# Optimization experiments

Hardware: AMD Instinct MI355X
Metric: run time of the kernel (lower is better)

The kernel has to match this reference:

```python
import jax, jax.numpy as jnp
import numpy as np

H, D_HEAD, MEM, K_OUT, J_DIM = 4, 16, 64, 192, 256
LN_EPS = 1e-5

def setup_inputs() -> dict:
    key = jax.random.key(0)
    ks = jax.random.split(key, 12)
    B, T, P = 4, 2048, 16
    inp = {
        "joint_repr": jax.random.normal(ks[0], (B, T, P, J_DIM), jnp.float32),
        "curvature": jax.random.uniform(ks[1], (B,), jnp.float32),
        "entropy": jax.random.uniform(ks[2], (B,), jnp.float32),
        "Wq": 0.02 * jax.random.normal(ks[3], (MEM, J_DIM), jnp.float32),
        "Wk": 0.02 * jax.random.normal(ks[4], (MEM, J_DIM), jnp.float32),
        "Wv": 0.02 * jax.random.normal(ks[5], (MEM, J_DIM), jnp.float32),
        "Wbeta_w": 0.05 * jax.random.normal(ks[6], (H, J_DIM), jnp.float32),
        "Wbeta_b": jnp.full((H,), 0.5, jnp.float32),
        "Walpha_w": 0.05 * jax.random.normal(ks[7], (H, J_DIM), jnp.float32),
        "Walpha_b": jnp.full((H,), -1.0, jnp.float32),
        "curv_w": 0.001 * jax.random.normal(ks[8], (H, 1), jnp.float32),
        "ent_w": 0.001 * jax.random.normal(ks[9], (H, 1), jnp.float32),
        "out_w": 0.01 * jax.random.normal(ks[10], (K_OUT, MEM), jnp.float32),
        "out_b": jnp.zeros((K_OUT,), jnp.float32),
        "ln_q_w": jnp.ones((D_HEAD,), jnp.float32),
        "ln_q_b": jnp.zeros((D_HEAD,), jnp.float32),
        "ln_k_w": jnp.ones((D_HEAD,), jnp.float32),
        "ln_k_b": jnp.zeros((D_HEAD,), jnp.float32),
    }
    return inp

def _ln(y, w, b):
    m = jnp.mean(y, axis=-1, keepdims=True)
    var = jnp.mean((y - m) ** 2, axis=-1, keepdims=True)
    return (y - m) / jnp.sqrt(var + LN_EPS) * w + b

def reference(joint_repr, curvature, entropy, Wq, Wk, Wv, Wbeta_w, Wbeta_b,
              Walpha_w, Walpha_b, curv_w, ent_w, out_w, out_b,
              ln_q_w, ln_q_b, ln_k_w, ln_k_b):
    B, T, P, J = joint_repr.shape
    N = B * P
    x = joint_repr.reshape(N, T, J)  # matches torch reshape(B*P, T, J)
    q = _ln((x @ Wq.T).reshape(N, T, H, D_HEAD), ln_q_w, ln_q_b)
    k = _ln((x @ Wk.T).reshape(N, T, H, D_HEAD), ln_k_w, ln_k_b)
    v = (x @ Wv.T).reshape(N, T, H, D_HEAD)
    k = k / jnp.clip(jnp.linalg.norm(k, axis=-1, keepdims=True), 1e-12)
    beta = jax.nn.sigmoid(x @ Wbeta_w.T + Wbeta_b)    # (N,T,H)
    alpha = jax.nn.sigmoid(x @ Walpha_w.T + Walpha_b)  # (N,T,H)
    # curvature modulation (detached in original)
    Kv = jnp.clip(jnp.abs(jax.lax.stop_gradient(curvature)), None, 10.0)
    Kv = jnp.repeat(Kv, P)  # (N,)
    beta = jax.nn.sigmoid(beta + Kv[:, None, None] * curv_w[:, 0])
    # entropy modulation (detached)
    Sv = jnp.clip(jax.lax.stop_gradient(entropy), 0.0, 5.0)
    Sv = jnp.repeat(Sv, P)
    alpha = jax.nn.sigmoid(alpha + Sv[:, None, None] * ent_w[:, 0])

    def step(M, inps):
        k_t, v_t, q_t, b_t, a_t = inps  # (N,H,d), (N,H)
        Mk = jnp.einsum('nhij,nhj->nhi', M, k_t)
        outer_kk = Mk[..., :, None] * k_t[..., None, :]
        outer_vk = v_t[..., :, None] * k_t[..., None, :]
        M = M - a_t[:, :, None, None] * outer_kk + b_t[:, :, None, None] * outer_vk
        o = jnp.einsum('nhij,nhj->nhi', M, q_t)
        return M, o

    M0 = jnp.zeros((N, H, D_HEAD, D_HEAD), joint_repr.dtype)
    xs = (k.transpose(1, 0, 2, 3), v.transpose(1, 0, 2, 3), q.transpose(1, 0, 2, 3),
          beta.transpose(1, 0, 2), alpha.transpose(1, 0, 2))
    _, outs = jax.lax.scan(step, M0, xs)  # (T,N,H,d)
    out = outs.transpose(1, 0, 2, 3).reshape(N, T, H * D_HEAD)
    fib = out @ out_w.T + out_b  # (N,T,K)
    return fib.reshape(B, P, T, K_OUT).transpose(0, 2, 1, 3)  # (B,T,P,K)
```

## Files before the change

kernel.cpp:

```cpp
#include <hip/hip_runtime.h>

#define TDIM 2048
#define SEG 16
#define SEGLEN 128

typedef __attribute__((ext_vector_type(8))) short short8;
typedef __attribute__((ext_vector_type(4))) short short4v;
typedef __attribute__((ext_vector_type(4))) float float4v;

__device__ __forceinline__ float sigf(float x) { return 1.0f / (1.0f + __expf(-x)); }

__device__ __forceinline__ unsigned short f2bf_rne(float f) {
    unsigned u = __float_as_uint(f);
    unsigned r = (u + 0x7fffu + ((u >> 16) & 1u)) >> 16;
    return (unsigned short)r;
}
__device__ __forceinline__ float bf2f(unsigned short h) {
    return __uint_as_float(((unsigned)h) << 16);
}
struct bfpair { short hi, lo; };
__device__ __forceinline__ bfpair cvt_split(float x) {
    bfpair p;
    unsigned short h = f2bf_rne(x);
    p.hi = (short)h;
    p.lo = (short)f2bf_rne(x - bf2f(h));
    return p;
}

__device__ __forceinline__ void split4_fast(float4 v, short4v& hi, short4v& lo) {
    unsigned h01, h23;
    asm("v_cvt_pk_bf16_f32 %0, %1, %2" : "=v"(h01) : "v"(v.x), "v"(v.y));
    asm("v_cvt_pk_bf16_f32 %0, %1, %2" : "=v"(h23) : "v"(v.z), "v"(v.w));
    float rx = v.x - __uint_as_float(h01 << 16);
    float ry = v.y - __uint_as_float(h01 & 0xffff0000u);
    float rz = v.z - __uint_as_float(h23 << 16);
    float rw = v.w - __uint_as_float(h23 & 0xffff0000u);
    unsigned l01, l23;
    asm("v_cvt_pk_bf16_f32 %0, %1, %2" : "=v"(l01) : "v"(rx), "v"(ry));
    asm("v_cvt_pk_bf16_f32 %0, %1, %2" : "=v"(l23) : "v"(rz), "v"(rw));
    union { unsigned u[2]; short4v s; } uh, ul;
    uh.u[0] = h01; uh.u[1] = h23;
    ul.u[0] = l01; ul.u[1] = l23;
    hi = uh.s; lo = ul.s;
}

template<int CTRL>
__device__ __forceinline__ float dpp_addt(float v) {
    int t = __builtin_amdgcn_update_dpp(0, __float_as_int(v), CTRL, 0xf, 0xf, true);
    return v + __int_as_float(t);
}
__device__ __forceinline__ float red16d(float v) {
    v = dpp_addt<0xB1>(v);
    v = dpp_addt<0x4E>(v);
    v = dpp_addt<0x141>(v);
    v = dpp_addt<0x140>(v);
    return v;
}

__device__ __forceinline__ float dot4f(float4 a, float4 b) {
    return fmaf(a.w, b.w, fmaf(a.z, b.z, fmaf(a.y, b.y, a.x * b.x)));
}
__device__ __forceinline__ float red4g(float v) {
    v += __shfl_xor(v, 16);
    v += __shfl_xor(v, 32);
    return v;
}

__device__ __forceinline__ void gld16(const void* g, void* l) {
    __builtin_amdgcn_global_load_lds(
        (const __attribute__((address_space(1))) unsigned*)g,
        (__attribute__((address_space(3))) unsigned*)l, 16, 0, 0);
}

__global__ __launch_bounds__(256) void prep_w_kernel(
    const float* __restrict__ Wq, const float* __restrict__ Wk, const float* __restrict__ Wv,
    const float* __restrict__ Wbw, const float* __restrict__ Waw,
    short* __restrict__ wimg)
{
    int u = blockIdx.x * 256 + threadIdx.x;
    if (u >= 6656) return;
    int kc = u / 1664, rem = u % 1664;
    int rr = rem >> 3, gg = rem & 7;
    const float* wrow = nullptr;
    if (rr < 64)       wrow = Wq  + (size_t)rr * 256;
    else if (rr < 128) wrow = Wk  + (size_t)(rr - 64) * 256;
    else if (rr < 192) wrow = Wv  + (size_t)(rr - 128) * 256;
    else if (rr < 196) wrow = Wbw + (size_t)(rr - 192) * 256;
    else if (rr < 200) wrow = Waw + (size_t)(rr - 196) * 256;
    int usw = (2 * gg) ^ (rr & 7);
    short* dh = wimg + ((size_t)kc * 3328 + rr * 16 + usw) * 8;
    short* dl = wimg + ((size_t)kc * 3328 + rr * 16 + (usw ^ 1)) * 8;
#pragma unroll
    for (int s = 0; s < 8; ++s) {
        float v = wrow ? wrow[kc * 64 + gg * 8 + s] : 0.0f;
        bfpair p = cvt_split(v);
        dh[s] = p.hi; dl[s] = p.lo;
    }
}

__global__ __launch_bounds__(256) void prep_ow_kernel(
    const float* __restrict__ ow, short* __restrict__ owimg)
{
    int u = blockIdx.x * 256 + threadIdx.x;
    if (u >= 1536) return;
    int rr = u >> 3, gg = u & 7;
    int usw = (2 * gg) ^ (rr & 7);
    short* dh = owimg + ((size_t)rr * 16 + usw) * 8;
    short* dl = owimg + ((size_t)rr * 16 + (usw ^ 1)) * 8;
#pragma unroll
    for (int s = 0; s < 8; ++s) {
        bfpair p = cvt_split(ow[(size_t)rr * 64 + gg * 8 + s]);
        dh[s] = p.hi; dl[s] = p.lo;
    }
}

__global__ __launch_bounds__(256, 4) void proj_kernel(
    const float* __restrict__ x, const float* __restrict__ curv, const float* __restrict__ ent,
    const short* __restrict__ wimg,
    const float* __restrict__ Wbb, const float* __restrict__ Wab,
    const float* __restrict__ cw, const float* __restrict__ ew,
    const float* __restrict__ lnqw, const float* __restrict__ lnqb,
    const float* __restrict__ lnkw, const float* __restrict__ lnkb,
    float* __restrict__ q_ws, float* __restrict__ k_ws, float* __restrict__ v_ws,
    float* __restrict__ beta_ws, float* __restrict__ alpha_ws)
{
    __shared__ __align__(16) short xsh[64 * 64];
    __shared__ __align__(16) short wsh[1664 * 8];

    const int tid = threadIdx.x;
    const int lane = tid & 63, wv = tid >> 6;
    const int i16 = lane & 15, gq = lane >> 4, swz = i16 & 7;
    const int row0 = blockIdx.x * 64;
    const int ntbase = (wv == 0) ? 0 : (1 + 3 * wv);
    const int ntcnt  = (wv == 0) ? 4 : 3;

    float4v acc[4][4];
#pragma unroll
    for (int m = 0; m < 4; ++m)
#pragma unroll
        for (int nI = 0; nI < 4; ++nI) acc[m][nI] = (float4v){0.f, 0.f, 0.f, 0.f};

    float4 xr[2];
#pragma unroll
    for (int it = 0; it < 2; ++it) {
        int f = it * 256 + tid, rr = f >> 3, c4 = f & 7;
        xr[it] = *(const float4*)&x[(size_t)(row0 + rr) * 256 + c4 * 4];
    }

    for (int hc = 0; hc < 8; ++hc) {
        __builtin_amdgcn_s_barrier();
        const short* wk = wimg + (size_t)(hc >> 1) * 26624;
        const int hoff = (hc & 1) * 8;
#pragma unroll
        for (int it = 0; it < 7; ++it) {
            int f = it * 256 + tid;
            if (f < 1664) {
                int rr = f >> 3, uu = f & 7;
                gld16(wk + ((size_t)rr * 16 + hoff + uu) * 8, &wsh[f * 8]);
            }
        }
        asm volatile("" ::: "memory");
#pragma unroll
        for (int it = 0; it < 2; ++it) {
            int f = it * 256 + tid, rr = f >> 3, c4 = f & 7;
            short4v hi, lo;
            split4_fast(xr[it], hi, lo);
            int usw = (2 * (c4 >> 1)) ^ (rr & 7);
            *(short4v*)&xsh[rr * 64 + usw * 8 + (c4 & 1) * 4] = hi;
            *(short4v*)&xsh[rr * 64 + (usw ^ 1) * 8 + (c4 & 1) * 4] = lo;
        }
        if (hc < 7) {
#pragma unroll
            for (int it = 0; it < 2; ++it) {
                int f = it * 256 + tid, rr = f >> 3, c4 = f & 7;
                xr[it] = *(const float4*)&x[(size_t)(row0 + rr) * 256 + (hc + 1) * 32 + c4 * 4];
            }
            asm volatile("s_waitcnt vmcnt(2) lgkmcnt(0)" ::: "memory");
        } else {
            asm volatile("s_waitcnt vmcnt(0) lgkmcnt(0)" ::: "memory");
        }
        __builtin_amdgcn_s_barrier();
        const int uA = ((2 * gq) ^ swz) * 8;
        short8 ah[4], al[4];
#pragma unroll
        for (int m = 0; m < 4; ++m) {
            const int rb = (m * 16 + i16) * 64;
            ah[m] = *(const short8*)&xsh[rb + uA];
            al[m] = *(const short8*)&xsh[rb + (uA ^ 8)];
        }
#pragma unroll
        for (int nI = 0; nI < 4; ++nI) if (nI < ntcnt) {
            const int rowB = ((ntbase + nI) * 16 + i16) * 64;
            short8 bh = *(const short8*)&wsh[rowB + uA];
            short8 bl = *(const short8*)&wsh[rowB + (uA ^ 8)];
#pragma unroll
            for (int m = 0; m < 4; ++m) {
                acc[m][nI] = __builtin_amdgcn_mfma_f32_16x16x32_bf16(ah[m], bh, acc[m][nI], 0, 0, 0);
                acc[m][nI] = __builtin_amdgcn_mfma_f32_16x16x32_bf16(ah[m], bl, acc[m][nI], 0, 0, 0);
                acc[m][nI] = __builtin_amdgcn_mfma_f32_16x16x32_bf16(al[m], bh, acc[m][nI], 0, 0, 0);
            }
        }
    }

    const int c = i16;
    const float lnqw_c = lnqw[c], lnqb_c = lnqb[c];
    const float lnkw_c = lnkw[c], lnkb_c = lnkb[c];
    const int nblk = row0 >> 11;
    const float Kv = fminf(fabsf(curv[nblk >> 4]), 10.0f);
    const float Sv = fminf(fmaxf(ent[nblk >> 4], 0.0f), 5.0f);
#pragma unroll
    for (int nI = 0; nI < 4; ++nI) if (nI < ntcnt) {
        const int nt = ntbase + nI;
#pragma unroll
        for (int m = 0; m < 4; ++m) {
#pragma unroll
            for (int j = 0; j < 4; ++j) {
                const int grow = row0 + m * 16 + gq * 4 + j;
                const int n = grow >> 11, t = grow & 2047;
                float y = acc[m][nI][j];
                if (nt < 4) {
                    float s = red16d(y), s2 = red16d(y * y);
                    float mean = s * 0.0625f;
                    float var = s2 * 0.0625f - mean * mean;
                    float inv = rsqrtf(var + 1e-5f);
                    q_ws[((size_t)(n * 4 + nt) * TDIM + t) * 16 + c] = (y - mean) * inv * lnqw_c + lnqb_c;
                } else if (nt < 8) {
                    float s = red16d(y), s2 = red16d(y * y);
                    float mean = s * 0.0625f;
                    float var = s2 * 0.0625f - mean * mean;
                    float inv = rsqrtf(var + 1e-5f);
                    float kn = (y - mean) * inv * lnkw_c + lnkb_c;
                    float s3 = red16d(kn * kn);
                    kn = kn / fmaxf(sqrtf(s3), 1e-12f);
                    k_ws[((size_t)(n * 4 + (nt - 4)) * TDIM + t) * 16 + c] = kn;
                } else if (nt < 12) {
                    v_ws[((size_t)(n * 4 + (nt - 8)) * TDIM + t) * 16 + c] = y;
                } else {
                    if (c < 4)
                        beta_ws[(size_t)(n * 4 + c) * TDIM + t] = sigf(sigf(y + Wbb[c]) + Kv * cw[c]);
                    else if (c < 8) {
                        int h = c - 4;
                        alpha_ws[(size_t)(n * 4 + h) * TDIM + t] = sigf(sigf(y + Wab[h]) + Sv * ew[h]);
                    }
                }
            }
        }
    }
}

__global__ __launch_bounds__(64) void scan_p1_kernel(
    const float* __restrict__ k_ws, const float* __restrict__ v_ws,
    const float* __restrict__ beta_ws, const float* __restrict__ alpha_ws,
    float* __restrict__ pq_ws)
{
    __shared__ __align__(16) float ks[128 * 16], bvs[128 * 16];
    __shared__ __align__(16) float tb1[128 * 4];
    const int tid = threadIdx.x;
    const int sid = blockIdx.x;
    const int cid = blockIdx.y;
    const int i = tid & 15, g = tid >> 4;
    const int t0g = sid * SEGLEN;
    const float* kb = k_ws + ((size_t)cid * TDIM + t0g) * 16;
    const float* vb = v_ws + ((size_t)cid * TDIM + t0g) * 16;
    const float* bb = beta_ws + (size_t)cid * TDIM + t0g;
    const float* ab = alpha_ws + (size_t)cid * TDIM + t0g;

    for (int f = tid; f < 128 * 16; f += 64) { ks[f] = 0.f; bvs[f] = 0.f; }
    for (int f = tid; f < 128 * 4; f += 64) tb1[f] = 0.f;
    __syncthreads();

    float4 kr[4], vr[4]; float be = 0.f, alp = 0.f;
    auto load_stage = [&](int s) {
        size_t t0 = (size_t)s * 64 + tid;
        const float4* kp = (const float4*)(kb + t0 * 16);
        const float4* vp = (const float4*)(vb + t0 * 16);
#pragma unroll
        for (int j = 0; j < 4; ++j) { kr[j] = kp[j]; vr[j] = vp[j]; }
        be = bb[t0]; alp = ab[t0];
    };
    auto commit_stage = [&](int s) {
        int r = (s & 1) * 64 + tid;
#pragma unroll
        for (int j = 0; j < 4; ++j) {
            *(float4*)&ks[r * 16 + 4 * j] = kr[j];
            float4 bv4 = make_float4(be * vr[j].x, be * vr[j].y, be * vr[j].z, be * vr[j].w);
            *(float4*)&bvs[r * 16 + 4 * j] = bv4;
        }
    };
    auto table_pass = [&](int s) {
        int r0 = (s & 1) * 64 + tid;
        int rm1 = (r0 - 1) & 127, rm2 = (r0 - 2) & 127;
        float C = 0.f, C2 = 0.f;
#pragma unroll
        for (int j = 0; j < 4; ++j) {
            float4 kt  = *(float4*)&ks[r0 * 16 + 4 * j];
            float4 km1 = *(float4*)&ks[rm1 * 16 + 4 * j];
            float4 km2 = *(float4*)&ks[rm2 * 16 + 4 * j];
            C  += dot4f(km1, kt);
            C2 += dot4f(km2, kt);
        }
        *(float4*)&tb1[r0 * 4] = make_float4(alp * C, alp * C2, alp, 0.f);
    };

    load_stage(0);
    commit_stage(0);
    __syncthreads();
    table_pass(0);
    __syncthreads();

    float4 Q4 = make_float4(0.f, 0.f, 0.f, 0.f);
    float4 P4 = make_float4(i == 4 * g + 0 ? 1.f : 0.f,
                            i == 4 * g + 1 ? 1.f : 0.f,
                            i == 4 * g + 2 ? 1.f : 0.f,
                            i == 4 * g + 3 ? 1.f : 0.f);
    float wq1 = 0.f, wq2 = 0.f, wp1 = 0.f, wp2 = 0.f;
    float4 k4m1 = make_float4(0.f, 0.f, 0.f, 0.f);
    float4 k4_0 = *(float4*)&ks[0 * 16 + 4 * g];
    float4 k4p1 = *(float4*)&ks[1 * 16 + 4 * g];
    float upQ_cur = 0.f;
    float upP_cur = ks[i];
    float4 ta0 = *(float4*)&tb1[0];
    float aC1_c = ta0.x, aC2_c = ta0.y, al_c = ta0.z;
    float bv_c = bvs[i];

    int t = 0;
    auto step = [&]() {
        int rp2 = (t + 2) & 127, rp1 = (t + 1) & 127;
        float4 k4in = *(float4*)&ks[rp2 * 16 + 4 * g];
        float4 tain = *(float4*)&tb1[rp1 * 4];
        float bvin = bvs[rp1 * 16 + i];
        float upQ = red4g(dot4f(Q4, k4p1));
        float upP = red4g(dot4f(P4, k4p1));
        Q4.x = fmaf(wq1, k4m1.x, Q4.x);
        Q4.y = fmaf(wq1, k4m1.y, Q4.y);
        Q4.z = fmaf(wq1, k4m1.z, Q4.z);
        Q4.w = fmaf(wq1, k4m1.w, Q4.w);
        P4.x = fmaf(wp1, k4m1.x, P4.x);
        P4.y = fmaf(wp1, k4m1.y, P4.y);
        P4.z = fmaf(wp1, k4m1.z, P4.z);
        P4.w = fmaf(wp1, k4m1.w, P4.w);
        float rq = fmaf(-aC2_c, wq2, fmaf(-al_c, upQ_cur, bv_c));
        float wq0 = fmaf(-aC1_c, wq1, rq);
        float rp_ = fmaf(-aC2_c, wp2, -al_c * upP_cur);
        float wp0 = fmaf(-aC1_c, wp1, rp_);
        wq2 = wq1; wq1 = wq0; wp2 = wp1; wp1 = wp0;
        k4m1 = k4_0; k4_0 = k4p1; k4p1 = k4in;
        upQ_cur = upQ; upP_cur = upP;
        aC1_c = tain.x; aC2_c = tain.y; al_c = tain.z; bv_c = bvin;
        ++t;
    };

    load_stage(1);
#pragma unroll 4
    for (int u = 0; u < 32; ++u) step();
    commit_stage(1);
#pragma unroll 4
    for (int u = 0; u < 16; ++u) step();
    table_pass(1);
#pragma unroll 4
    for (int u = 0; u < 16; ++u) step();
#pragma unroll 4
    for (int u = 0; u < 64; ++u) step();

    Q4.x = fmaf(wq1, k4m1.x, Q4.x);
    Q4.y = fmaf(wq1, k4m1.y, Q4.y);
    Q4.z = fmaf(wq1, k4m1.z, Q4.z);
    Q4.w = fmaf(wq1, k4m1.w, Q4.w);
    P4.x = fmaf(wp1, k4m1.x, P4.x);
    P4.y = fmaf(wp1, k4m1.y, P4.y);
    P4.z = fmaf(wp1, k4m1.z, P4.z);
    P4.w = fmaf(wp1, k4m1.w, P4.w);

    float* dst = pq_ws + ((size_t)cid * 15 + sid) * 512;
    *(float4*)&dst[i * 16 + 4 * g] = Q4;
    *(float4*)&dst[256 + i * 16 + 4 * g] = P4;
}

__global__ __launch_bounds__(64) void scan_p2_kernel(
    const float* __restrict__ pq_ws, float* __restrict__ min_ws)
{
    __shared__ float Mlds[256], Plds[256];
    const int tid = threadIdx.x;
    const int cid = blockIdx.x;
    const int i = tid & 15, g = tid >> 4;
    float4 M4 = make_float4(0.f, 0.f, 0.f, 0.f);
    *(float4*)&min_ws[((size_t)cid * SEG + 0) * 256 + i * 16 + 4 * g] = M4;
    for (int sid = 0; sid < 15; ++sid) {
        const float* base = pq_ws + ((size_t)cid * 15 + sid) * 512;
        float4 Qn = *(const float4*)&base[i * 16 + 4 * g];
        float4 Pn = *(const float4*)&base[256 + i * 16 + 4 * g];
        *(float4*)&Mlds[i * 16 + 4 * g] = M4;
        *(float4*)&Plds[i * 16 + 4 * g] = Pn;
        __syncthreads();
        float4 acc = Qn;
#pragma unroll
        for (int m = 0; m < 16; ++m) {
            float mm = Mlds[i * 16 + m];
            float4 pr = *(float4*)&Plds[m * 16 + 4 * g];
            acc.x = fmaf(mm, pr.x, acc.x);
            acc.y = fmaf(mm, pr.y, acc.y);
            acc.z = fmaf(mm, pr.z, acc.z);
            acc.w = fmaf(mm, pr.w, acc.w);
        }
        M4 = acc;
        __syncthreads();
        *(float4*)&min_ws[((size_t)cid * SEG + sid + 1) * 256 + i * 16 + 4 * g] = M4;
    }
}

__global__ __launch_bounds__(64) void scan_p3_kernel(
    const float* __restrict__ q_ws, const float* __restrict__ k_ws, const float* __restrict__ v_ws,
    const float* __restrict__ beta_ws, const float* __restrict__ alpha_ws,
    const float* __restrict__ min_ws, float* __restrict__ o_ws)
{
    __shared__ __align__(16) float ks[128 * 16], qs[128 * 16], bvs[128 * 16];
    __shared__ __align__(16) float tbl[128 * 8];
    __shared__ __align__(16) float os[64 * 16];
    const int tid = threadIdx.x;
    const int sid = blockIdx.x;
    const int cid = blockIdx.y;
    const int i = tid & 15, g = tid >> 4;
    const int t0g = sid * SEGLEN;
    const float* kb = k_ws + ((size_t)cid * TDIM + t0g) * 16;
    const float* qb = q_ws + ((size_t)cid * TDIM + t0g) * 16;
    const float* vb = v_ws + ((size_t)cid * TDIM + t0g) * 16;
    const float* bb = beta_ws + (size_t)cid * TDIM + t0g;
    const float* ab = alpha_ws + (size_t)cid * TDIM + t0g;
    float* obp = o_ws + ((size_t)cid * TDIM + t0g) * 16;

    for (int f = tid; f < 128 * 16; f += 64) { ks[f] = 0.f; qs[f] = 0.f; bvs[f] = 0.f; }
    for (int f = tid; f < 128 * 8; f += 64) tbl[f] = 0.f;
    __syncthreads();

    float4 kr[4], qr[4], vr[4]; float be = 0.f, alp = 0.f;
    auto load_stage = [&](int s) {
        size_t t0 = (size_t)s * 64 + tid;
        const float4* kp = (const float4*)(kb + t0 * 16);
        const float4* qp = (const float4*)(qb + t0 * 16);
        const float4* vp = (const float4*)(vb + t0 * 16);
#pragma unroll
        for (int j = 0; j < 4; ++j) { kr[j] = kp[j]; qr[j] = qp[j]; vr[j] = vp[j]; }
        be = bb[t0]; alp = ab[t0];
    };
    auto commit_stage = [&](int s) {
        int r = (s & 1) * 64 + tid;
#pragma unroll
        for (int j = 0; j < 4; ++j) {
            *(float4*)&ks[r * 16 + 4 * j] = kr[j];
            *(float4*)&qs[r * 16 + 4 * j] = qr[j];
            float4 bv4 = make_float4(be * vr[j].x, be * vr[j].y, be * vr[j].z, be * vr[j].w);
            *(float4*)&bvs[r * 16 + 4 * j] = bv4;
        }
    };
    auto table_pass = [&](int s) {
        int r0 = (s & 1) * 64 + tid;
        int rm1 = (r0 - 1) & 127, rm2 = (r0 - 2) & 127;
        float C = 0.f, C2 = 0.f, d = 0.f, e = 0.f, E2 = 0.f;
#pragma unroll
        for (int j = 0; j < 4; ++j) {
            float4 kt  = *(float4*)&ks[r0 * 16 + 4 * j];
            float4 km1 = *(float4*)&ks[rm1 * 16 + 4 * j];
            float4 km2 = *(float4*)&ks[rm2 * 16 + 4 * j];
            float4 qt  = *(float4*)&qs[r0 * 16 + 4 * j];
            C  += dot4f(km1, kt);
            C2 += dot4f(km2, kt);
            d  += dot4f(kt,  qt);
            e  += dot4f(km1, qt);
            E2 += dot4f(km2, qt);
        }
        *(float4*)&tbl[r0 * 8] = make_float4(alp * C, alp * C2, d, e);
        *(float2*)&tbl[r0 * 8 + 4] = make_float2(E2, alp);
    };

    load_stage(0);
    commit_stage(0);
    __syncthreads();
    table_pass(0);
    __syncthreads();

    float4 M4 = *(const float4*)&min_ws[((size_t)cid * SEG + sid) * 256 + i * 16 + 4 * g];
    float w1 = 0.f, w2 = 0.f;
    float4 k4m1 = make_float4(0.f, 0.f, 0.f, 0.f);
    float4 k4_0 = *(float4*)&ks[0 * 16 + 4 * g];
    float4 q4_0 = *(float4*)&qs[0 * 16 + 4 * g];
    float4 k4p1 = *(float4*)&ks[1 * 16 + 4 * g];
    float4 q4p1 = *(float4*)&qs[1 * 16 + 4 * g];
    float up_cur = red4g(dot4f(M4, k4_0));
    float rp_cur = red4g(dot4f(M4, q4_0));
    float4 ta0 = *(float4*)&tbl[0];
    float aC1_c = ta0.x, aC2_c = ta0.y, d_c = ta0.z, e_c = ta0.w;
    float2 tx0 = *(float2*)&tbl[4];
    float E2_c = tx0.x, al_c = tx0.y;
    float bv_c = bvs[i];

    int t = 0;
    auto step = [&]() {
        int rp2 = (t + 2) & 127, rp1 = (t + 1) & 127;
        float4 k4in = *(float4*)&ks[rp2 * 16 + 4 * g];
        float4 q4in = *(float4*)&qs[rp2 * 16 + 4 * g];
        float4 tain = *(float4*)&tbl[rp1 * 8];
        float2 txin = *(float2*)&tbl[rp1 * 8 + 4];
        float bvin = bvs[rp1 * 16 + i];
        float up = red4g(dot4f(M4, k4p1));
        float rp = red4g(dot4f(M4, q4p1));
        M4.x = fmaf(w1, k4m1.x, M4.x);
        M4.y = fmaf(w1, k4m1.y, M4.y);
        M4.z = fmaf(w1, k4m1.z, M4.z);
        M4.w = fmaf(w1, k4m1.w, M4.w);
        float r = fmaf(-aC2_c, w2, fmaf(-al_c, up_cur, bv_c));
        float w0 = fmaf(-aC1_c, w1, r);
        float o = fmaf(w0, d_c, fmaf(w1, e_c, fmaf(w2, E2_c, rp_cur)));
        if (g == 0) os[(t & 63) * 16 + i] = o;
        w2 = w1; w1 = w0;
        k4m1 = k4_0; k4_0 = k4p1; k4p1 = k4in;
        q4p1 = q4in;
        up_cur = up; rp_cur = rp;
        aC1_c = tain.x; aC2_c = tain.y; d_c = tain.z; e_c = tain.w;
        E2_c = txin.x; al_c = txin.y; bv_c = bvin;
        ++t;
    };

    for (int s = 0; s < 2; ++s) {
        if (s == 0) load_stage(1);
#pragma unroll 4
        for (int u = 0; u < 32; ++u) step();
        if (s == 0) commit_stage(1);
#pragma unroll 4
        for (int u = 0; u < 16; ++u) step();
        if (s == 0) table_pass(1);
#pragma unroll 4
        for (int u = 0; u < 16; ++u) step();
#pragma unroll
        for (int j = 0; j < 4; ++j) {
            float4 ov = *(float4*)&os[(tid * 4 + j) * 4];
            *(float4*)&obp[(size_t)s * 1024 + (tid * 4 + j) * 4] = ov;
        }
    }
}

__global__ __launch_bounds__(256, 4) void outproj_kernel(
    const float* __restrict__ o_ws, const short* __restrict__ owimg,
    const float* __restrict__ ob, float* __restrict__ out)
{
    __shared__ __align__(16) short osh[64 * 64];
    __shared__ __align__(16) short wsh[1536 * 8];
    const int tid = threadIdx.x;
    const int lane = tid & 63, wv = tid >> 6;
    const int i16 = lane & 15, gq = lane >> 4, swz = i16 & 7;
    const int row0 = blockIdx.x * 64;
    const int ntbase = wv * 3;

    float4v acc[4][3];
#pragma unroll
    for (int m = 0; m < 4; ++m)
#pragma unroll
        for (int nI = 0; nI < 3; ++nI) acc[m][nI] = (float4v){0.f, 0.f, 0.f, 0.f};

    float4 orr[2];
#pragma unroll
    for (int it = 0; it < 2; ++it) {
        int f = it * 256 + tid, rr = f >> 3, c4 = f & 7;
        int grow = row0 + rr;
        int n = grow >> 11, t = grow & 2047;
        int h = c4 >> 2, d4 = c4 & 3;
        orr[it] = *(const float4*)&o_ws[((size_t)(n * 4 + h) * TDIM + t) * 16 + d4 * 4];
    }

#pragma unroll
    for (int half = 0; half < 2; ++half) {
        __builtin_amdgcn_s_barrier();
#pragma unroll
        for (int it = 0; it < 6; ++it) {
            int f = it * 256 + tid;
            int rr = f >> 3, uu = f & 7;
            gld16(owimg + ((size_t)rr * 16 + half * 8 + uu) * 8, &wsh[f * 8]);
        }
        asm volatile("" ::: "memory");
#pragma unroll
        for (int it = 0; it < 2; ++it) {
            int f = it * 256 + tid, rr = f >> 3, c4 = f & 7;
            short4v hi, lo;
            split4_fast(orr[it], hi, lo);
            int usw = (2 * (c4 >> 1)) ^ (rr & 7);
            *(short4v*)&osh[rr * 64 + usw * 8 + (c4 & 1) * 4] = hi;
            *(short4v*)&osh[rr * 64 + (usw ^ 1) * 8 + (c4 & 1) * 4] = lo;
        }
        if (half == 0) {
#pragma unroll
            for (int it = 0; it < 2; ++it) {
                int f = it * 256 + tid, rr = f >> 3, c4 = f & 7;
                int grow = row0 + rr;
                int n = grow >> 11, t = grow & 2047;
                int col = 32 + c4 * 4;
                int h = col >> 4, d4 = (col >> 2) & 3;
                orr[it] = *(const float4*)&o_ws[((size_t)(n * 4 + h) * TDIM + t) * 16 + d4 * 4];
            }
            asm volatile("s_waitcnt vmcnt(2) lgkmcnt(0)" ::: "memory");
        } else {
            asm volatile("s_waitcnt vmcnt(0) lgkmcnt(0)" ::: "memory");
        }
        __builtin_amdgcn_s_barrier();

        const int uA = ((2 * gq) ^ swz) * 8;
        short8 ah[4], al[4];
#pragma unroll
        for (int m = 0; m < 4; ++m) {
            const int rb = (m * 16 + i16) * 64;
            ah[m] = *(const short8*)&osh[rb + uA];
            al[m] = *(const short8*)&osh[rb + (uA ^ 8)];
        }
#pragma unroll
        for (int nI = 0; nI < 3; ++nI) {
            const int rowB = ((ntbase + nI) * 16 + i16) * 64;
            short8 bh = *(const short8*)&wsh[rowB + uA];
            short8 bl = *(const short8*)&wsh[rowB + (uA ^ 8)];
#pragma unroll
            for (int m = 0; m < 4; ++m) {
                acc[m][nI] = __builtin_amdgcn_mfma_f32_16x16x32_bf16(ah[m], bh, acc[m][nI], 0, 0, 0);
                acc[m][nI] = __builtin_amdgcn_mfma_f32_16x16x32_bf16(ah[m], bl, acc[m][nI], 0, 0, 0);
                acc[m][nI] = __builtin_amdgcn_mfma_f32_16x16x32_bf16(al[m], bh, acc[m][nI], 0, 0, 0);
            }
        }
    }

#pragma unroll
    for (int nI = 0; nI < 3; ++nI) {
        const int nt = ntbase + nI;
        const float bias = ob[nt * 16 + i16];
#pragma unroll
        for (int m = 0; m < 4; ++m) {
#pragma unroll
            for (int j = 0; j < 4; ++j) {
                int grow = row0 + m * 16 + gq * 4 + j;
                int n = grow >> 11, t = grow & 2047;
                int b = n >> 4, p = n & 15;
                out[((size_t)(b * TDIM + t) * 16 + p) * 192 + nt * 16 + i16] = acc[m][nI][j] + bias;
            }
        }
    }
}

extern "C" void kernel_launch(void* const* d_in, const int* in_sizes, int n_in,
                              void* d_out, int out_size, void* d_ws, size_t ws_size,
                              hipStream_t stream) {
    (void)in_sizes; (void)n_in; (void)out_size; (void)ws_size;
    const float* x    = (const float*)d_in[0];
    const float* curv = (const float*)d_in[1];
    const float* ent  = (const float*)d_in[2];
    const float* Wq   = (const float*)d_in[3];
    const float* Wk   = (const float*)d_in[4];
    const float* Wv   = (const float*)d_in[5];
    const float* Wbw  = (const float*)d_in[6];
    const float* Wbb  = (const float*)d_in[7];
    const float* Waw  = (const float*)d_in[8];
    const float* Wab  = (const float*)d_in[9];
    const float* cw   = (const float*)d_in[10];
    const float* ew   = (const float*)d_in[11];
    const float* ow   = (const float*)d_in[12];
    const float* ob   = (const float*)d_in[13];
    const float* lnqw = (const float*)d_in[14];
    const float* lnqb = (const float*)d_in[15];
    const float* lnkw = (const float*)d_in[16];
    const float* lnkb = (const float*)d_in[17];
    float* out = (float*)d_out;

    float* ws = (float*)d_ws;
    float* q_ws     = ws;
    float* k_ws     = q_ws + 8388608;
    float* v_ws     = k_ws + 8388608;
    float* beta_ws  = v_ws + 8388608;
    float* alpha_ws = beta_ws + 524288;
    float* o_ws     = alpha_ws + 524288;

    short* wimg  = (short*)o_ws;
    short* owimg = (short*)q_ws;
    float* pq_ws  = out;
    float* min_ws = out + 1966080;

    prep_w_kernel<<<26, 256, 0, stream>>>(Wq, Wk, Wv, Wbw, Waw, wimg);
    proj_kernel<<<2048, 256, 0, stream>>>(x, curv, ent, wimg, Wbb, Wab,
                                          cw, ew, lnqw, lnqb, lnkw, lnkb,
                                          q_ws, k_ws, v_ws, beta_ws, alpha_ws);
    scan_p1_kernel<<<dim3(15, 256), 64, 0, stream>>>(k_ws, v_ws, beta_ws, alpha_ws, pq_ws);
    scan_p2_kernel<<<256, 64, 0, stream>>>(pq_ws, min_ws);
    scan_p3_kernel<<<dim3(16, 256), 64, 0, stream>>>(q_ws, k_ws, v_ws, beta_ws, alpha_ws,
                                                     min_ws, o_ws);
    prep_ow_kernel<<<6, 256, 0, stream>>>(ow, owimg);
    outproj_kernel<<<2048, 256, 0, stream>>>(o_ws, owimg, ob, out);
}
```

Measured before the change: 516.2 us.

## Halve scan segment length to 64 and double GEMM block rows to 128

The chunked delta-rule scan now splits the 2048-step sequence into 32 segments of 64 steps instead of 16 of 128. This doubles the number of parallel blocks in phases 1 and 3, halves the serial chain per block, and removes the two-stage load pipelining inside each segment, at the cost of a longer serial prefix combine in phase 2. Separately, the projection and output-projection GEMM kernels move to 512-thread blocks covering 128 rows, so each loaded weight tile is reused across two row groups of waves. Workspace offsets are adjusted to match the larger number of partial states.

```diff
diff --git a/kernel.cpp b/kernel.cpp
--- a/kernel.cpp
+++ b/kernel.cpp
@@ -1,8 +1,8 @@
 #include <hip/hip_runtime.h>
 
 #define TDIM 2048
-#define SEG 16
-#define SEGLEN 128
+#define SEGN 32
+#define SEGL 64
 
 typedef __attribute__((ext_vector_type(8))) short short8;
 typedef __attribute__((ext_vector_type(4))) short short4v;
@@ -114,7 +114,7 @@
     }
 }
 
-__global__ __launch_bounds__(256, 4) void proj_kernel(
+__global__ __launch_bounds__(512, 4) void proj_kernel(
     const float* __restrict__ x, const float* __restrict__ curv, const float* __restrict__ ent,
     const short* __restrict__ wimg,
     const float* __restrict__ Wbb, const float* __restrict__ Wab,
@@ -124,15 +124,16 @@
     float* __restrict__ q_ws, float* __restrict__ k_ws, float* __restrict__ v_ws,
     float* __restrict__ beta_ws, float* __restrict__ alpha_ws)
 {
-    __shared__ __align__(16) short xsh[64 * 64];
+    __shared__ __align__(16) short xsh[128 * 64];
     __shared__ __align__(16) short wsh[1664 * 8];
 
     const int tid = threadIdx.x;
     const int lane = tid & 63, wv = tid >> 6;
     const int i16 = lane & 15, gq = lane >> 4, swz = i16 & 7;
-    const int row0 = blockIdx.x * 64;
-    const int ntbase = (wv == 0) ? 0 : (1 + 3 * wv);
-    const int ntcnt  = (wv == 0) ? 4 : 3;
+    const int row0 = blockIdx.x * 128;
+    const int wr = wv >> 2, wc = wv & 3;
+    const int ntbase = (wc == 0) ? 0 : (1 + 3 * wc);
+    const int ntcnt  = (wc == 0) ? 4 : 3;
 
     float4v acc[4][4];
 #pragma unroll
@@ -143,7 +144,7 @@
     float4 xr[2];
 #pragma unroll
     for (int it = 0; it < 2; ++it) {
-        int f = it * 256 + tid, rr = f >> 3, c4 = f & 7;
+        int f = it * 512 + tid, rr = f >> 3, c4 = f & 7;
         xr[it] = *(const float4*)&x[(size_t)(row0 + rr) * 256 + c4 * 4];
     }
 
@@ -152,8 +153,8 @@
         const short* wk = wimg + (size_t)(hc >> 1) * 26624;
         const int hoff = (hc & 1) * 8;
 #pragma unroll
-        for (int it = 0; it < 7; ++it) {
-            int f = it * 256 + tid;
+        for (int it = 0; it < 4; ++it) {
+            int f = it * 512 + tid;
             if (f < 1664) {
                 int rr = f >> 3, uu = f & 7;
                 gld16(wk + ((size_t)rr * 16 + hoff + uu) * 8, &wsh[f * 8]);
@@ -162,7 +163,7 @@
         asm volatile("" ::: "memory");
 #pragma unroll
         for (int it = 0; it < 2; ++it) {
-            int f = it * 256 + tid, rr = f >> 3, c4 = f & 7;
+            int f = it * 512 + tid, rr = f >> 3, c4 = f & 7;
             short4v hi, lo;
             split4_fast(xr[it], hi, lo);
             int usw = (2 * (c4 >> 1)) ^ (rr & 7);
@@ -172,7 +173,7 @@
         if (hc < 7) {
 #pragma unroll
             for (int it = 0; it < 2; ++it) {
-                int f = it * 256 + tid, rr = f >> 3, c4 = f & 7;
+                int f = it * 512 + tid, rr = f >> 3, c4 = f & 7;
                 xr[it] = *(const float4*)&x[(size_t)(row0 + rr) * 256 + (hc + 1) * 32 + c4 * 4];
             }
             asm volatile("s_waitcnt vmcnt(2) lgkmcnt(0)" ::: "memory");
@@ -184,7 +185,7 @@
         short8 ah[4], al[4];
 #pragma unroll
         for (int m = 0; m < 4; ++m) {
-            const int rb = (m * 16 + i16) * 64;
+            const int rb = (wr * 64 + m * 16 + i16) * 64;
             ah[m] = *(const short8*)&xsh[rb + uA];
             al[m] = *(const short8*)&xsh[rb + (uA ^ 8)];
         }
@@ -215,7 +216,7 @@
         for (int m = 0; m < 4; ++m) {
 #pragma unroll
             for (int j = 0; j < 4; ++j) {
-                const int grow = row0 + m * 16 + gq * 4 + j;
+                const int grow = row0 + wr * 64 + m * 16 + gq * 4 + j;
                 const int n = grow >> 11, t = grow & 2047;
                 float y = acc[m][nI][j];
                 if (nt < 4) {
@@ -248,48 +249,46 @@
     }
 }
 
+
 __global__ __launch_bounds__(64) void scan_p1_kernel(
     const float* __restrict__ k_ws, const float* __restrict__ v_ws,
     const float* __restrict__ beta_ws, const float* __restrict__ alpha_ws,
     float* __restrict__ pq_ws)
 {
-    __shared__ __align__(16) float ks[128 * 16], bvs[128 * 16];
-    __shared__ __align__(16) float tb1[128 * 4];
+    __shared__ __align__(16) float ks[68 * 16], bvs[68 * 16];
+    __shared__ __align__(16) float tb1[68 * 4];
     const int tid = threadIdx.x;
     const int sid = blockIdx.x;
     const int cid = blockIdx.y;
     const int i = tid & 15, g = tid >> 4;
-    const int t0g = sid * SEGLEN;
+    const int t0g = sid * SEGL;
     const float* kb = k_ws + ((size_t)cid * TDIM + t0g) * 16;
     const float* vb = v_ws + ((size_t)cid * TDIM + t0g) * 16;
     const float* bb = beta_ws + (size_t)cid * TDIM + t0g;
     const float* ab = alpha_ws + (size_t)cid * TDIM + t0g;
 
-    for (int f = tid; f < 128 * 16; f += 64) { ks[f] = 0.f; bvs[f] = 0.f; }
-    for (int f = tid; f < 128 * 4; f += 64) tb1[f] = 0.f;
+    for (int f = tid; f < 68 * 16; f += 64) { ks[f] = 0.f; bvs[f] = 0.f; }
+    for (int f = tid; f < 68 * 4; f += 64) tb1[f] = 0.f;
     __syncthreads();
 
-    float4 kr[4], vr[4]; float be = 0.f, alp = 0.f;
-    auto load_stage = [&](int s) {
-        size_t t0 = (size_t)s * 64 + tid;
-        const float4* kp = (const float4*)(kb + t0 * 16);
-        const float4* vp = (const float4*)(vb + t0 * 16);
-#pragma unroll
-        for (int j = 0; j < 4; ++j) { kr[j] = kp[j]; vr[j] = vp[j]; }
-        be = bb[t0]; alp = ab[t0];
-    };
-    auto commit_stage = [&](int s) {
-        int r = (s & 1) * 64 + tid;
+    {
+        const float4* kp = (const float4*)(kb + (size_t)tid * 16);
+        const float4* vp = (const float4*)(vb + (size_t)tid * 16);
+        float be = bb[tid];
+        int r = tid + 2;
 #pragma unroll
         for (int j = 0; j < 4; ++j) {
-            *(float4*)&ks[r * 16 + 4 * j] = kr[j];
-            float4 bv4 = make_float4(be * vr[j].x, be * vr[j].y, be * vr[j].z, be * vr[j].w);
+            float4 kv = kp[j];
+            float4 vv = vp[j];
+            *(float4*)&ks[r * 16 + 4 * j] = kv;
+            float4 bv4 = make_float4(be * vv.x, be * vv.y, be * vv.z, be * vv.w);
             *(float4*)&bvs[r * 16 + 4 * j] = bv4;
         }
-    };
-    auto table_pass = [&](int s) {
-        int r0 = (s & 1) * 64 + tid;
-        int rm1 = (r0 - 1) & 127, rm2 = (r0 - 2) & 127;
+    }
+    float alp = ab[tid];
+    __syncthreads();
+    {
+        int r0 = tid + 2, rm1 = tid + 1, rm2 = tid;
         float C = 0.f, C2 = 0.f;
 #pragma unroll
         for (int j = 0; j < 4; ++j) {
@@ -300,12 +299,7 @@
             C2 += dot4f(km2, kt);
         }
         *(float4*)&tb1[r0 * 4] = make_float4(alp * C, alp * C2, alp, 0.f);
-    };
-
-    load_stage(0);
-    commit_stage(0);
-    __syncthreads();
-    table_pass(0);
+    }
     __syncthreads();
 
     float4 Q4 = make_float4(0.f, 0.f, 0.f, 0.f);
@@ -315,20 +309,20 @@
                             i == 4 * g + 3 ? 1.f : 0.f);
     float wq1 = 0.f, wq2 = 0.f, wp1 = 0.f, wp2 = 0.f;
     float4 k4m1 = make_float4(0.f, 0.f, 0.f, 0.f);
-    float4 k4_0 = *(float4*)&ks[0 * 16 + 4 * g];
-    float4 k4p1 = *(float4*)&ks[1 * 16 + 4 * g];
+    float4 k4_0 = *(float4*)&ks[2 * 16 + 4 * g];
+    float4 k4p1 = *(float4*)&ks[3 * 16 + 4 * g];
     float upQ_cur = 0.f;
-    float upP_cur = ks[i];
-    float4 ta0 = *(float4*)&tb1[0];
+    float upP_cur = ks[2 * 16 + i];
+    float4 ta0 = *(float4*)&tb1[2 * 4];
     float aC1_c = ta0.x, aC2_c = ta0.y, al_c = ta0.z;
-    float bv_c = bvs[i];
+    float bv_c = bvs[2 * 16 + i];
 
     int t = 0;
     auto step = [&]() {
-        int rp2 = (t + 2) & 127, rp1 = (t + 1) & 127;
-        float4 k4in = *(float4*)&ks[rp2 * 16 + 4 * g];
-        float4 tain = *(float4*)&tb1[rp1 * 4];
-        float bvin = bvs[rp1 * 16 + i];
+        int rin = t + 4, rtb = t + 3;
+        float4 k4in = *(float4*)&ks[rin * 16 + 4 * g];
+        float4 tain = *(float4*)&tb1[rtb * 4];
+        float bvin = bvs[rtb * 16 + i];
         float upQ = red4g(dot4f(Q4, k4p1));
         float upP = red4g(dot4f(P4, k4p1));
         Q4.x = fmaf(wq1, k4m1.x, Q4.x);
@@ -350,15 +344,6 @@
         ++t;
     };
 
-    load_stage(1);
-#pragma unroll 4
-    for (int u = 0; u < 32; ++u) step();
-    commit_stage(1);
-#pragma unroll 4
-    for (int u = 0; u < 16; ++u) step();
-    table_pass(1);
-#pragma unroll 4
-    for (int u = 0; u < 16; ++u) step();
 #pragma unroll 4
     for (int u = 0; u < 64; ++u) step();
 
@@ -371,7 +356,7 @@
     P4.z = fmaf(wp1, k4m1.z, P4.z);
     P4.w = fmaf(wp1, k4m1.w, P4.w);
 
-    float* dst = pq_ws + ((size_t)cid * 15 + sid) * 512;
+    float* dst = pq_ws + ((size_t)cid * 31 + sid) * 512;
     *(float4*)&dst[i * 16 + 4 * g] = Q4;
     *(float4*)&dst[256 + i * 16 + 4 * g] = P4;
 }
@@ -384,9 +369,9 @@
     const int cid = blockIdx.x;
     const int i = tid & 15, g = tid >> 4;
     float4 M4 = make_float4(0.f, 0.f, 0.f, 0.f);
-    *(float4*)&min_ws[((size_t)cid * SEG + 0) * 256 + i * 16 + 4 * g] = M4;
-    for (int sid = 0; sid < 15; ++sid) {
-        const float* base = pq_ws + ((size_t)cid * 15 + sid) * 512;
+    *(float4*)&min_ws[((size_t)cid * SEGN + 0) * 256 + i * 16 + 4 * g] = M4;
+    for (int sid = 0; sid < 31; ++sid) {
+        const float* base = pq_ws + ((size_t)cid * 31 + sid) * 512;
         float4 Qn = *(const float4*)&base[i * 16 + 4 * g];
         float4 Pn = *(const float4*)&base[256 + i * 16 + 4 * g];
         *(float4*)&Mlds[i * 16 + 4 * g] = M4;
@@ -404,7 +389,7 @@
         }
         M4 = acc;
         __syncthreads();
-        *(float4*)&min_ws[((size_t)cid * SEG + sid + 1) * 256 + i * 16 + 4 * g] = M4;
+        *(float4*)&min_ws[((size_t)cid * SEGN + sid + 1) * 256 + i * 16 + 4 * g] = M4;
     }
 }
 
@@ -413,14 +398,14 @@
     const float* __restrict__ beta_ws, const float* __restrict__ alpha_ws,
     const float* __restrict__ min_ws, float* __restrict__ o_ws)
 {
-    __shared__ __align__(16) float ks[128 * 16], qs[128 * 16], bvs[128 * 16];
-    __shared__ __align__(16) float tbl[128 * 8];
+    __shared__ __align__(16) float ks[68 * 16], qs[68 * 16], bvs[68 * 16];
+    __shared__ __align__(16) float tbl[68 * 8];
     __shared__ __align__(16) float os[64 * 16];
     const int tid = threadIdx.x;
     const int sid = blockIdx.x;
     const int cid = blockIdx.y;
     const int i = tid & 15, g = tid >> 4;
-    const int t0g = sid * SEGLEN;
+    const int t0g = sid * SEGL;
     const float* kb = k_ws + ((size_t)cid * TDIM + t0g) * 16;
     const float* qb = q_ws + ((size_t)cid * TDIM + t0g) * 16;
     const float* vb = v_ws + ((size_t)cid * TDIM + t0g) * 16;
@@ -428,33 +413,31 @@
     const float* ab = alpha_ws + (size_t)cid * TDIM + t0g;
     float* obp = o_ws + ((size_t)cid * TDIM + t0g) * 16;
 
-    for (int f = tid; f < 128 * 16; f += 64) { ks[f] = 0.f; qs[f] = 0.f; bvs[f] = 0.f; }
-    for (int f = tid; f < 128 * 8; f += 64) tbl[f] = 0.f;
+    for (int f = tid; f < 68 * 16; f += 64) { ks[f] = 0.f; qs[f] = 0.f; bvs[f] = 0.f; }
+    for (int f = tid; f < 68 * 8; f += 64) tbl[f] = 0.f;
     __syncthreads();
 
-    float4 kr[4], qr[4], vr[4]; float be = 0.f, alp = 0.f;
-    auto load_stage = [&](int s) {
-        size_t t0 = (size_t)s * 64 + tid;
-        const float4* kp = (const float4*)(kb + t0 * 16);
-        const float4* qp = (const float4*)(qb + t0 * 16);
-        const float4* vp = (const float4*)(vb + t0 * 16);
-#pragma unroll
-        for (int j = 0; j < 4; ++j) { kr[j] = kp[j]; qr[j] = qp[j]; vr[j] = vp[j]; }
-        be = bb[t0]; alp = ab[t0];
-    };
-    auto commit_stage = [&](int s) {
-        int r = (s & 1) * 64 + tid;
+    {
+        const float4* kp = (const float4*)(kb + (size_t)tid * 16);
+        const float4* qp = (const float4*)(qb + (size_t)tid * 16);
+        const float4* vp = (const float4*)(vb + (size_t)tid * 16);
+        float be = bb[tid];
+        int r = tid + 2;
 #pragma unroll
         for (int j = 0; j < 4; ++j) {
-            *(float4*)&ks[r * 16 + 4 * j] = kr[j];
-            *(float4*)&qs[r * 16 + 4 * j] = qr[j];
-            float4 bv4 = make_float4(be * vr[j].x, be * vr[j].y, be * vr[j].z, be * vr[j].w);
+            float4 kv = kp[j];
+            float4 qv = qp[j];
+            float4 vv = vp[j];
+            *(float4*)&ks[r * 16 + 4 * j] = kv;
+            *(float4*)&qs[r * 16 + 4 * j] = qv;
+            float4 bv4 = make_float4(be * vv.x, be * vv.y, be * vv.z, be * vv.w);
             *(float4*)&bvs[r * 16 + 4 * j] = bv4;
         }
-    };
-    auto table_pass = [&](int s) {
-        int r0 = (s & 1) * 64 + tid;
-        int rm1 = (r0 - 1) & 127, rm2 = (r0 - 2) & 127;
+    }
+    float alp = ab[tid];
+    __syncthreads();
+    {
+        int r0 = tid + 2, rm1 = tid + 1, rm2 = tid;
         float C = 0.f, C2 = 0.f, d = 0.f, e = 0.f, E2 = 0.f;
 #pragma unroll
         for (int j = 0; j < 4; ++j) {
@@ -470,37 +453,32 @@
         }
         *(float4*)&tbl[r0 * 8] = make_float4(alp * C, alp * C2, d, e);
         *(float2*)&tbl[r0 * 8 + 4] = make_float2(E2, alp);
-    };
-
-    load_stage(0);
-    commit_stage(0);
+    }
     __syncthreads();
-    table_pass(0);
-    __syncthreads();
-
-    float4 M4 = *(const float4*)&min_ws[((size_t)cid * SEG + sid) * 256 + i * 16 + 4 * g];
+
+    float4 M4 = *(const float4*)&min_ws[((size_t)cid * SEGN + sid) * 256 + i * 16 + 4 * g];
     float w1 = 0.f, w2 = 0.f;
     float4 k4m1 = make_float4(0.f, 0.f, 0.f, 0.f);
-    float4 k4_0 = *(float4*)&ks[0 * 16 + 4 * g];
-    float4 q4_0 = *(float4*)&qs[0 * 16 + 4 * g];
-    float4 k4p1 = *(float4*)&ks[1 * 16 + 4 * g];
-    float4 q4p1 = *(float4*)&qs[1 * 16 + 4 * g];
+    float4 k4_0 = *(float4*)&ks[2 * 16 + 4 * g];
+    float4 q4_0 = *(float4*)&qs[2 * 16 + 4 * g];
+    float4 k4p1 = *(float4*)&ks[3 * 16 + 4 * g];
+    float4 q4p1 = *(float4*)&qs[3 * 16 + 4 * g];
     float up_cur = red4g(dot4f(M4, k4_0));
     float rp_cur = red4g(dot4f(M4, q4_0));
-    float4 ta0 = *(float4*)&tbl[0];
+    float4 ta0 = *(float4*)&tbl[2 * 8];
     float aC1_c = ta0.x, aC2_c = ta0.y, d_c = ta0.z, e_c = ta0.w;
-    float2 tx0 = *(float2*)&tbl[4];
+    float2 tx0 = *(float2*)&tbl[2 * 8 + 4];
     float E2_c = tx0.x, al_c = tx0.y;
-    float bv_c = bvs[i];
+    float bv_c = bvs[2 * 16 + i];
 
     int t = 0;
     auto step = [&]() {
-        int rp2 = (t + 2) & 127, rp1 = (t + 1) & 127;
-        float4 k4in = *(float4*)&ks[rp2 * 16 + 4 * g];
-        float4 q4in = *(float4*)&qs[rp2 * 16 + 4 * g];
-        float4 tain = *(float4*)&tbl[rp1 * 8];
-        float2 txin = *(float2*)&tbl[rp1 * 8 + 4];
-        float bvin = bvs[rp1 * 16 + i];
+        int rin = t + 4, rtb = t + 3;
+        float4 k4in = *(float4*)&ks[rin * 16 + 4 * g];
+        float4 q4in = *(float4*)&qs[rin * 16 + 4 * g];
+        float4 tain = *(float4*)&tbl[rtb * 8];
+        float2 txin = *(float2*)&tbl[rtb * 8 + 4];
+        float bvin = bvs[rtb * 16 + i];
         float up = red4g(dot4f(M4, k4p1));
         float rp = red4g(dot4f(M4, q4p1));
         M4.x = fmaf(w1, k4m1.x, M4.x);
@@ -510,7 +488,7 @@
         float r = fmaf(-aC2_c, w2, fmaf(-al_c, up_cur, bv_c));
         float w0 = fmaf(-aC1_c, w1, r);
         float o = fmaf(w0, d_c, fmaf(w1, e_c, fmaf(w2, E2_c, rp_cur)));
-        if (g == 0) os[(t & 63) * 16 + i] = o;
+        if (g == 0) os[t * 16 + i] = o;
         w2 = w1; w1 = w0;
         k4m1 = k4_0; k4_0 = k4p1; k4p1 = k4in;
         q4p1 = q4in;
@@ -520,35 +498,28 @@
         ++t;
     };
 
-    for (int s = 0; s < 2; ++s) {
-        if (s == 0) load_stage(1);
 #pragma unroll 4
-        for (int u = 0; u < 32; ++u) step();
-        if (s == 0) commit_stage(1);
-#pragma unroll 4
-        for (int u = 0; u < 16; ++u) step();
-        if (s == 0) table_pass(1);
-#pragma unroll 4
-        for (int u = 0; u < 16; ++u) step();
-#pragma unroll
-        for (int j = 0; j < 4; ++j) {
-            float4 ov = *(float4*)&os[(tid * 4 + j) * 4];
-            *(float4*)&obp[(size_t)s * 1024 + (tid * 4 + j) * 4] = ov;
-        }
-    }
-}
-
-__global__ __launch_bounds__(256, 4) void outproj_kernel(
+    for (int u = 0; u < 64; ++u) step();
+
+#pragma unroll
+    for (int j = 0; j < 4; ++j) {
+        float4 ov = *(float4*)&os[(tid * 4 + j) * 4];
+        *(float4*)&obp[(tid * 4 + j) * 4] = ov;
+    }
+}
+
+__global__ __launch_bounds__(512, 4) void outproj_kernel(
     const float* __restrict__ o_ws, const short* __restrict__ owimg,
     const float* __restrict__ ob, float* __restrict__ out)
 {
-    __shared__ __align__(16) short osh[64 * 64];
+    __shared__ __align__(16) short osh[128 * 64];
     __shared__ __align__(16) short wsh[1536 * 8];
     const int tid = threadIdx.x;
     const int lane = tid & 63, wv = tid >> 6;
     const int i16 = lane & 15, gq = lane >> 4, swz = i16 & 7;
-    const int row0 = blockIdx.x * 64;
-    const int ntbase = wv * 3;
+    const int row0 = blockIdx.x * 128;
+    const int wr = wv >> 2, wc = wv & 3;
+    const int ntbase = wc * 3;
 
     float4v acc[4][3];
 #pragma unroll
@@ -559,7 +530,7 @@
     float4 orr[2];
 #pragma unroll
     for (int it = 0; it < 2; ++it) {
-        int f = it * 256 + tid, rr = f >> 3, c4 = f & 7;
+        int f = it * 512 + tid, rr = f >> 3, c4 = f & 7;
         int grow = row0 + rr;
         int n = grow >> 11, t = grow & 2047;
         int h = c4 >> 2, d4 = c4 & 3;
@@ -570,15 +541,15 @@
     for (int half = 0; half < 2; ++half) {
         __builtin_amdgcn_s_barrier();
 #pragma unroll
-        for (int it = 0; it < 6; ++it) {
-            int f = it * 256 + tid;
+        for (int it = 0; it < 3; ++it) {
+            int f = it * 512 + tid;
             int rr = f >> 3, uu = f & 7;
             gld16(owimg + ((size_t)rr * 16 + half * 8 + uu) * 8, &wsh[f * 8]);
         }
         asm volatile("" ::: "memory");
 #pragma unroll
         for (int it = 0; it < 2; ++it) {
-            int f = it * 256 + tid, rr = f >> 3, c4 = f & 7;
+            int f = it * 512 + tid, rr = f >> 3, c4 = f & 7;
             short4v hi, lo;
             split4_fast(orr[it], hi, lo);
             int usw = (2 * (c4 >> 1)) ^ (rr & 7);
@@ -588,7 +559,7 @@
         if (half == 0) {
 #pragma unroll
             for (int it = 0; it < 2; ++it) {
-                int f = it * 256 + tid, rr = f >> 3, c4 = f & 7;
+                int f = it * 512 + tid, rr = f >> 3, c4 = f & 7;
                 int grow = row0 + rr;
                 int n = grow >> 11, t = grow & 2047;
                 int col = 32 + c4 * 4;
@@ -605,7 +576,7 @@
         short8 ah[4], al[4];
 #pragma unroll
         for (int m = 0; m < 4; ++m) {
-            const int rb = (m * 16 + i16) * 64;
+            const int rb = (wr * 64 + m * 16 + i16) * 64;
             ah[m] = *(const short8*)&osh[rb + uA];
             al[m] = *(const short8*)&osh[rb + (uA ^ 8)];
         }
@@ -631,7 +602,7 @@
         for (int m = 0; m < 4; ++m) {
 #pragma unroll
             for (int j = 0; j < 4; ++j) {
-                int grow = row0 + m * 16 + gq * 4 + j;
+                int grow = row0 + wr * 64 + m * 16 + gq * 4 + j;
                 int n = grow >> 11, t = grow & 2047;
                 int b = n >> 4, p = n & 15;
                 out[((size_t)(b * TDIM + t) * 16 + p) * 192 + nt * 16 + i16] = acc[m][nI][j] + bias;
@@ -675,16 +646,16 @@
     short* wimg  = (short*)o_ws;
     short* owimg = (short*)q_ws;
     float* pq_ws  = out;
-    float* min_ws = out + 1966080;
+    float* min_ws = out + 4063232;
 
     prep_w_kernel<<<26, 256, 0, stream>>>(Wq, Wk, Wv, Wbw, Waw, wimg);
-    proj_kernel<<<2048, 256, 0, stream>>>(x, curv, ent, wimg, Wbb, Wab,
+    proj_kernel<<<1024, 512, 0, stream>>>(x, curv, ent, wimg, Wbb, Wab,
                                           cw, ew, lnqw, lnqb, lnkw, lnkb,
                                           q_ws, k_ws, v_ws, beta_ws, alpha_ws);
-    scan_p1_kernel<<<dim3(15, 256), 64, 0, stream>>>(k_ws, v_ws, beta_ws, alpha_ws, pq_ws);
+    scan_p1_kernel<<<dim3(31, 256), 64, 0, stream>>>(k_ws, v_ws, beta_ws, alpha_ws, pq_ws);
     scan_p2_kernel<<<256, 64, 0, stream>>>(pq_ws, min_ws);
-    scan_p3_kernel<<<dim3(16, 256), 64, 0, stream>>>(q_ws, k_ws, v_ws, beta_ws, alpha_ws,
+    scan_p3_kernel<<<dim3(32, 256), 64, 0, stream>>>(q_ws, k_ws, v_ws, beta_ws, alpha_ws,
                                                      min_ws, o_ws);
     prep_ow_kernel<<<6, 256, 0, stream>>>(ow, owimg);
-    outproj_kernel<<<2048, 256, 0, stream>>>(o_ws, owimg, ob, out);
-}
+    outproj_kernel<<<1024, 512, 0, stream>>>(o_ws, owimg, ob, out);
+}
```

Result: faster. 471.1 us (-8.8%).
